# Kernel tuning notes

Measured on AMD Instinct MI355X. Metric: run time of the kernel, lower is better.

The kernel has to match this reference:

```python
import jax, jax.numpy as jnp
import numpy as np
from jax import lax

NPOINT = 1024
NSAMPLE = 64
RADIUS = 0.2
EPS = 1e-5  # BatchNorm eps


def farthest_point_sample(xyz, npoint):
    # xyz: [B, N, 3] -> idx [B, npoint]; deterministic init at point 0
    B, N, _ = xyz.shape

    def step(carry, _):
        dist, farthest = carry
        centroid = jnp.take_along_axis(xyz, farthest[:, None, None], axis=1)  # [B,1,3]
        d = jnp.sum((xyz - centroid) ** 2, axis=-1)  # [B,N]
        dist = jnp.minimum(dist, d)
        new_far = jnp.argmax(dist, axis=-1).astype(jnp.int32)
        return (dist, new_far), farthest

    init = (jnp.full((B, N), 1e10, xyz.dtype), jnp.zeros((B,), jnp.int32))
    _, idxs = lax.scan(step, init, None, length=npoint)
    return jnp.transpose(idxs)  # [B, npoint]


def square_distance(src, dst):
    # src [B,S,3], dst [B,N,3] -> [B,S,N]
    d = -2.0 * jnp.einsum('bsc,bnc->bsn', src, dst)
    d += jnp.sum(src ** 2, -1)[:, :, None]
    d += jnp.sum(dst ** 2, -1)[:, None, :]
    return d


def query_ball_point(radius, nsample, xyz, new_xyz):
    B, N, _ = xyz.shape
    sqr = square_distance(new_xyz, xyz)  # [B,S,N]
    gi = jnp.where(sqr > radius ** 2, N, jnp.arange(N, dtype=jnp.int32))
    gi = jnp.sort(gi, axis=-1)[:, :, :nsample]  # [B,S,K]
    first = gi[:, :, :1]
    gi = jnp.where(gi == N, first, gi)
    return gi


def mlp_bn_relu(x, W, g, b):
    # x [B,S,K,Cin], W [Cin,Cout]; 1x1 conv + training-mode BN + ReLU
    y = jnp.einsum('bskc,co->bsko', x, W)
    m = jnp.mean(y, axis=(0, 1, 2))
    v = jnp.var(y, axis=(0, 1, 2))
    y = (y - m) * lax.rsqrt(v + EPS) * g + b
    return jax.nn.relu(y)


def setup_inputs() -> dict:
    key = jax.random.key(0)
    ks = jax.random.split(key, 8)
    B, N, C = 8, 4096, 128
    xyz = jax.random.uniform(ks[0], (B, N, 3), dtype=jnp.float32)
    features = jax.random.normal(ks[1], (B, C, N), dtype=jnp.float32)
    c_in = C + 3  # use_xyz
    W1 = jax.random.normal(ks[2], (c_in, 128), dtype=jnp.float32) * 0.05
    W2 = jax.random.normal(ks[3], (128, 128), dtype=jnp.float32) * 0.05
    W3 = jax.random.normal(ks[4], (128, 256), dtype=jnp.float32) * 0.05
    return {
        'xyz': xyz, 'features': features,
        'W1': W1, 'g1': jnp.ones((128,)), 'b1': jnp.zeros((128,)),
        'W2': W2, 'g2': jnp.ones((128,)), 'b2': jnp.zeros((128,)),
        'W3': W3, 'g3': jnp.ones((256,)), 'b3': jnp.zeros((256,)),
    }


def reference(xyz, features, W1, g1, b1, W2, g2, b2, W3, g3, b3):
    fps_idx = farthest_point_sample(xyz, NPOINT)              # [B,S]
    new_xyz = jnp.take_along_axis(xyz, fps_idx[:, :, None], axis=1)  # [B,S,3]
    gi = query_ball_point(RADIUS, NSAMPLE, xyz, new_xyz)      # [B,S,K]
    gather = jax.vmap(lambda p, i: p[i])                      # per-batch gather
    grouped_xyz = gather(xyz, gi) - new_xyz[:, :, None, :]    # [B,S,K,3]
    grouped_feat = gather(jnp.transpose(features, (0, 2, 1)), gi)  # [B,S,K,C]
    x = jnp.concatenate([grouped_xyz, grouped_feat], axis=-1)  # [B,S,K,3+C]
    x = mlp_bn_relu(x, W1, g1, b1)
    x = mlp_bn_relu(x, W2, g2, b2)
    x = mlp_bn_relu(x, W3, g3, b3)
    new_features = jnp.transpose(jnp.max(x, axis=2), (0, 2, 1))  # [B,256,S]
    return new_xyz, new_features
```

## Files before the change

### kernel.cpp

```cpp
#include <hip/hip_runtime.h>

#define B_  8
#define N_  4096
#define S_  1024
#define K_  64
#define CF_ 128
#define M_  (B_*S_*K_)

typedef __attribute__((ext_vector_type(8))) short bshort8;
typedef __attribute__((ext_vector_type(4))) float f32x4;
typedef __attribute__((ext_vector_type(4))) int   i32x4;
typedef __attribute__((ext_vector_type(2))) float f32x2;

__device__ __forceinline__ unsigned short f2bf(float f){
  unsigned int u = __float_as_uint(f);
  u = u + 0x7FFFu + ((u >> 16) & 1u);
  return (unsigned short)(u >> 16);
}
__device__ __forceinline__ float bf2f(unsigned short h){
  return __uint_as_float(((unsigned int)h) << 16);
}

#define DPP_PAIR_STEP(CTRL)                                                     \
  {                                                                             \
    int _vi = __builtin_amdgcn_update_dpp(__float_as_int(best), __float_as_int(best), (CTRL), 0xF, 0xF, false); \
    int _ii = __builtin_amdgcn_update_dpp(bidx, bidx, (CTRL), 0xF, 0xF, false); \
    float _ov = __int_as_float(_vi);                                            \
    bool _tk = (_ov > best) || (_ov == best && _ii < bidx);                     \
    best = _tk ? _ov : best;                                                    \
    bidx = _tk ? _ii : bidx;                                                    \
  }

__global__ __launch_bounds__(256) void fps_kernel(const float* __restrict__ xyz,
                                                  float* __restrict__ nx_out,
                                                  float* __restrict__ nx_ws){
#pragma clang fp contract(off)
  __shared__ float sx[N_], sy[N_], sz[N_];
  __shared__ int   sidx[S_];
  __shared__ alignas(16) float redv[2][4];
  __shared__ alignas(16) int   redi[2][4];
  const int b = blockIdx.x, t = threadIdx.x;
  const int lane = t & 63, w = t >> 6;
  const float* xb = xyz + (size_t)b*N_*3;
  f32x2 px[8], py[8], pz[8], dist[8];
#pragma unroll
  for (int j=0;j<8;++j){
    int i0 = (2*j)*256 + t, i1 = (2*j+1)*256 + t;
    float x0=xb[i0*3+0], y0=xb[i0*3+1], z0=xb[i0*3+2];
    float x1=xb[i1*3+0], y1=xb[i1*3+1], z1=xb[i1*3+2];
    px[j] = (f32x2){x0,x1}; py[j] = (f32x2){y0,y1}; pz[j] = (f32x2){z0,z1};
    dist[j] = (f32x2){1e10f,1e10f};
    sx[i0]=x0; sy[i0]=y0; sz[i0]=z0;
    sx[i1]=x1; sy[i1]=y1; sz[i1]=z1;
  }
  __syncthreads();
  int farthest = 0;
  for (int it=0; it<S_; ++it){
    if (t==0) sidx[it] = farthest;
    float cx = sx[farthest], cy = sy[farthest], cz = sz[farthest];
    f32x2 cx2 = (f32x2){cx,cx}, cy2 = (f32x2){cy,cy}, cz2 = (f32x2){cz,cz};
    float best = -1.0f; int bidx = 0;
#pragma unroll
    for (int j=0;j<8;++j){
      f32x2 dx = px[j] - cx2;
      f32x2 dy = py[j] - cy2;
      f32x2 dz = pz[j] - cz2;
      f32x2 d  = (dx*dx + dy*dy) + dz*dz;
      f32x2 nd;
      nd.x = fminf(dist[j].x, d.x);
      nd.y = fminf(dist[j].y, d.y);
      dist[j] = nd;
      bool tk0 = nd.x > best;
      best = tk0 ? nd.x : best;
      bidx = tk0 ? ((2*j)*256 + t) : bidx;
      bool tk1 = nd.y > best;
      best = tk1 ? nd.y : best;
      bidx = tk1 ? ((2*j+1)*256 + t) : bidx;
    }
    DPP_PAIR_STEP(0xB1);
    DPP_PAIR_STEP(0x4E);
    DPP_PAIR_STEP(0x124);
    DPP_PAIR_STEP(0x128);
    DPP_PAIR_STEP(0x142);
    DPP_PAIR_STEP(0x143);
    const int buf = it & 1;
    if (lane == 63){ redv[buf][w] = best; redi[buf][w] = bidx; }
    __syncthreads();
    f32x4 vv = *(const f32x4*)&redv[buf][0];
    i32x4 iv = *(const i32x4*)&redi[buf][0];
    float v01 = vv[0]; int i01 = iv[0];
    { bool tk = (vv[1] > v01) || (vv[1] == v01 && iv[1] < i01); v01 = tk?vv[1]:v01; i01 = tk?iv[1]:i01; }
    float v23 = vv[2]; int i23 = iv[2];
    { bool tk = (vv[3] > v23) || (vv[3] == v23 && iv[3] < i23); v23 = tk?vv[3]:v23; i23 = tk?iv[3]:i23; }
    { bool tk = (v23 > v01) || (v23 == v01 && i23 < i01); v01 = tk?v23:v01; i01 = tk?i23:i01; }
    farthest = i01;
  }
  __syncthreads();
  for (int i=t; i<S_; i+=256){
    int id = sidx[i];
    size_t base = (size_t)(b*S_+i)*3;
    float vx=sx[id], vy=sy[id], vz=sz[id];
    nx_out[base+0]=vx; nx_out[base+1]=vy; nx_out[base+2]=vz;
    nx_ws[base+0]=vx;  nx_ws[base+1]=vy;  nx_ws[base+2]=vz;
  }
}

__global__ __launch_bounds__(256) void qbp_kernel(const float* __restrict__ xyz,
                                                  const float* __restrict__ nx,
                                                  int* __restrict__ gi){
  const double R2 = 0.2*0.2;
  int gtid = blockIdx.x*256 + threadIdx.x;
  int wid = gtid >> 6, lane = gtid & 63;
  int b = wid >> 10, s = wid & 1023;
  const float* xb = xyz + (size_t)b*N_*3;
  const float* c  = nx + (size_t)(b*S_+s)*3;
  double cx=(double)c[0], cy=(double)c[1], cz=(double)c[2];
  double cc = cx*cx + cy*cy + cz*cz;
  int* g = gi + (size_t)(b*S_+s)*K_;
  int count = 0, first = -1;
  for (int ch=0; ch<64 && count<K_; ++ch){
    int i = ch*64 + lane;
    double x = (double)xb[i*3+0], y = (double)xb[i*3+1], z = (double)xb[i*3+2];
    double e  = cx*x + cy*y + cz*z;
    double pp = x*x + y*y + z*z;
    double d  = -2.0*e + cc + pp;
    bool keep = !(d > R2);
    unsigned long long bal = __ballot(keep);
    int pos = count + __builtin_popcountll(bal & ((1ull<<lane)-1ull));
    if (keep && pos < K_) g[pos] = i;
    if (first < 0 && bal) first = ch*64 + (int)__builtin_ctzll(bal);
    count += __builtin_popcountll(bal);
  }
  if (count < K_){
    int p = count + lane;
    if (p < K_) g[p] = first;
  }
}

__global__ __launch_bounds__(256) void transpose_kernel(const float* __restrict__ f,
                                                        unsigned short* __restrict__ ft){
  __shared__ float tile[32][33];
  int b = blockIdx.z, ct = blockIdx.y, nt = blockIdx.x;
  int tx = threadIdx.x & 31, ty = threadIdx.x >> 5;
#pragma unroll
  for (int r=0; r<32; r+=8)
    tile[ty+r][tx] = f[((size_t)(b*128 + ct*32 + ty + r))*4096 + nt*32 + tx];
  __syncthreads();
#pragma unroll
  for (int r=0; r<32; r+=8){
    int n = nt*32 + ty + r, cc = ct*32 + tx;
    ft[((size_t)b*4096 + n)*128 + cc] = f2bf(tile[tx][ty+r]);
  }
}

__global__ void wprep_kernel(const float* __restrict__ W1, const float* __restrict__ W2,
                             const float* __restrict__ W3,
                             unsigned short* __restrict__ Wt1, unsigned short* __restrict__ Wt2,
                             unsigned short* __restrict__ Wt3){
  int t = blockIdx.x*blockDim.x + threadIdx.x;
  int stride = gridDim.x*blockDim.x;
  for (int idx=t; idx<128*160; idx+=stride){
    int n = idx/160, k = idx-(idx/160)*160;
    float v = 0.f;
    if (k < 128) v = W1[(k+3)*128 + n];
    else if (k < 131) v = W1[(k-128)*128 + n];
    Wt1[idx] = f2bf(v);
  }
  for (int idx=t; idx<128*128; idx+=stride){
    int n = idx>>7, k = idx&127;
    Wt2[idx] = f2bf(W2[k*128+n]);
  }
  for (int idx=t; idx<256*128; idx+=stride){
    int n = idx>>7, k = idx&127;
    Wt3[idx] = f2bf(W3[k*256+n]);
  }
}

template<int PHASE>
__global__ __launch_bounds__(256,2) void mm_fused(
    const unsigned short* __restrict__ featT,
    const unsigned short* __restrict__ Wt1,
    const unsigned short* __restrict__ Wt2,
    const unsigned short* __restrict__ Wt3,
    const int* __restrict__ gi,
    const float* __restrict__ xyz,
    const float* __restrict__ nxyz,
    const float* __restrict__ ss1,
    const float* __restrict__ ss2,
    float* __restrict__ slots,
    float* __restrict__ minv,
    float* __restrict__ maxv)
{
  __shared__ alignas(16) unsigned short At[128*40];
  __shared__ alignas(16) unsigned short Bt[128*40];
  __shared__ alignas(16) unsigned short Y[(PHASE>=2)?(128*136):16];
  __shared__ int giL[128];

  const int t = threadIdx.x;
  const int mblk = blockIdx.x;
  const int b = mblk >> 9;
  const int lane = t&63, wave = t>>6;
  const int wm = wave>>1, wn = wave&1;
  const int lrow = lane&15, quad = lane>>4;
  const int slot = mblk & 63;

  if (t<128) giL[t] = gi[(size_t)mblk*128 + t];
  __syncthreads();

  f32x4 acc[4][4];
  const f32x4 z4 = {0.f,0.f,0.f,0.f};
#pragma unroll
  for (int i=0;i<4;++i)
#pragma unroll
    for (int j=0;j<4;++j) acc[i][j]=z4;

  for (int ch=0; ch<5; ++ch){
#pragma unroll
    for (int half=0; half<2; ++half){
      int sl = t + half*256; int r = sl>>2, p = sl&3;
      *(bshort8*)&Bt[r*40+p*8] = *(const bshort8*)(Wt1 + r*160 + ch*32 + p*8);
      if (ch < 4){
        int i = giL[r];
        *(bshort8*)&At[r*40+p*8] =
            *(const bshort8*)(featT + ((size_t)b*N_ + i)*CF_ + ch*32 + p*8);
      } else {
        union { bshort8 v; unsigned short u[8]; } o;
#pragma unroll
        for (int e=0;e<8;++e) o.u[e]=0;
        if (p==0){
          int i = giL[r];
          int s = ((mblk*128 + r) >> 6) & 1023;
          const float* pp = xyz  + ((size_t)b*N_ + i)*3;
          const float* qq = nxyz + (size_t)(b*S_ + s)*3;
          o.u[0] = f2bf(__fsub_rn(pp[0],qq[0]));
          o.u[1] = f2bf(__fsub_rn(pp[1],qq[1]));
          o.u[2] = f2bf(__fsub_rn(pp[2],qq[2]));
        }
        *(bshort8*)&At[r*40+p*8] = o.v;
      }
    }
    __syncthreads();
    bshort8 af[4], bfr[4];
#pragma unroll
    for (int mt=0; mt<4; ++mt) af[mt]  = *(const bshort8*)&At[(wm*64+mt*16+lrow)*40 + quad*8];
#pragma unroll
    for (int nt=0; nt<4; ++nt) bfr[nt] = *(const bshort8*)&Bt[(wn*64+nt*16+lrow)*40 + quad*8];
#pragma unroll
    for (int mt=0; mt<4; ++mt)
#pragma unroll
      for (int nt=0; nt<4; ++nt)
        acc[mt][nt] = __builtin_amdgcn_mfma_f32_16x16x32_bf16(af[mt], bfr[nt], acc[mt][nt], 0,0,0);
    __syncthreads();
  }

  if constexpr (PHASE==1){
#pragma unroll
    for (int nt=0; nt<4; ++nt){
      float s=0.f, s2=0.f;
#pragma unroll
      for (int mt=0; mt<4; ++mt)
#pragma unroll
        for (int r=0; r<4; ++r){ float v=acc[mt][nt][r]; s+=v; s2=fmaf(v,v,s2); }
      s  += __shfl_xor(s,16,64);  s  += __shfl_xor(s,32,64);
      s2 += __shfl_xor(s2,16,64); s2 += __shfl_xor(s2,32,64);
      if (lane<16){
        int c = wn*64+nt*16+lane;
        atomicAdd(&slots[(slot*128+c)*2+0], s);
        atomicAdd(&slots[(slot*128+c)*2+1], s2);
      }
    }
    return;
  }

  if constexpr (PHASE>=2){
#pragma unroll
    for (int nt=0; nt<4; ++nt){
      int c = wn*64+nt*16+lrow;
      float sc = ss1[c], sh = ss1[128+c];
#pragma unroll
      for (int mt=0; mt<4; ++mt)
#pragma unroll
        for (int r=0; r<4; ++r){
          int row = wm*64+mt*16+quad*4+r;
          Y[row*136 + c] = f2bf(fmaxf(fmaf(acc[mt][nt][r], sc, sh), 0.f));
        }
    }
    __syncthreads();

#pragma unroll
    for (int i=0;i<4;++i)
#pragma unroll
      for (int j=0;j<4;++j) acc[i][j]=z4;
    for (int ch=0; ch<4; ++ch){
#pragma unroll
      for (int half=0; half<2; ++half){
        int sl = t + half*256; int r = sl>>2, p = sl&3;
        *(bshort8*)&Bt[r*40+p*8] = *(const bshort8*)(Wt2 + r*128 + ch*32 + p*8);
      }
      __syncthreads();
      bshort8 af[4], bfr[4];
#pragma unroll
      for (int mt=0; mt<4; ++mt) af[mt]  = *(const bshort8*)&Y[(wm*64+mt*16+lrow)*136 + ch*32 + quad*8];
#pragma unroll
      for (int nt=0; nt<4; ++nt) bfr[nt] = *(const bshort8*)&Bt[(wn*64+nt*16+lrow)*40 + quad*8];
#pragma unroll
      for (int mt=0; mt<4; ++mt)
#pragma unroll
        for (int nt=0; nt<4; ++nt)
          acc[mt][nt] = __builtin_amdgcn_mfma_f32_16x16x32_bf16(af[mt], bfr[nt], acc[mt][nt], 0,0,0);
      __syncthreads();
    }
  }

  if constexpr (PHASE==2){
#pragma unroll
    for (int nt=0; nt<4; ++nt){
      float s=0.f, s2=0.f;
#pragma unroll
      for (int mt=0; mt<4; ++mt)
#pragma unroll
        for (int r=0; r<4; ++r){ float v=acc[mt][nt][r]; s+=v; s2=fmaf(v,v,s2); }
      s  += __shfl_xor(s,16,64);  s  += __shfl_xor(s,32,64);
      s2 += __shfl_xor(s2,16,64); s2 += __shfl_xor(s2,32,64);
      if (lane<16){
        int c = wn*64+nt*16+lane;
        atomicAdd(&slots[(slot*128+c)*2+0], s);
        atomicAdd(&slots[(slot*128+c)*2+1], s2);
      }
    }
    return;
  }

  if constexpr (PHASE==3){
#pragma unroll
    for (int nt=0; nt<4; ++nt){
      int c = wn*64+nt*16+lrow;
      float sc = ss2[c], sh = ss2[128+c];
#pragma unroll
      for (int mt=0; mt<4; ++mt)
#pragma unroll
        for (int r=0; r<4; ++r){
          int row = wm*64+mt*16+quad*4+r;
          Y[row*136 + c] = f2bf(fmaxf(fmaf(acc[mt][nt][r], sc, sh), 0.f));
        }
    }
    __syncthreads();

    for (int h=0; h<2; ++h){
#pragma unroll
      for (int i=0;i<4;++i)
#pragma unroll
        for (int j=0;j<4;++j) acc[i][j]=z4;
      for (int ch=0; ch<4; ++ch){
#pragma unroll
        for (int half=0; half<2; ++half){
          int sl = t + half*256; int r = sl>>2, p = sl&3;
          *(bshort8*)&Bt[r*40+p*8] =
              *(const bshort8*)(Wt3 + ((size_t)(h*128+r))*128 + ch*32 + p*8);
        }
        __syncthreads();
        bshort8 af[4], bfr[4];
#pragma unroll
        for (int mt=0; mt<4; ++mt) af[mt]  = *(const bshort8*)&Y[(wm*64+mt*16+lrow)*136 + ch*32 + quad*8];
#pragma unroll
        for (int nt=0; nt<4; ++nt) bfr[nt] = *(const bshort8*)&Bt[(wn*64+nt*16+lrow)*40 + quad*8];
#pragma unroll
        for (int mt=0; mt<4; ++mt)
#pragma unroll
          for (int nt=0; nt<4; ++nt)
            acc[mt][nt] = __builtin_amdgcn_mfma_f32_16x16x32_bf16(af[mt], bfr[nt], acc[mt][nt], 0,0,0);
        __syncthreads();
      }
#pragma unroll
      for (int nt=0; nt<4; ++nt){
        float s=0.f, s2=0.f, mx=-3.0e38f, mn=3.0e38f;
#pragma unroll
        for (int mt=0; mt<4; ++mt)
#pragma unroll
          for (int r=0; r<4; ++r){
            float v=acc[mt][nt][r];
            s+=v; s2=fmaf(v,v,s2);
            mx=fmaxf(mx,v); mn=fminf(mn,v);
          }
        s  += __shfl_xor(s,16,64);  s  += __shfl_xor(s,32,64);
        s2 += __shfl_xor(s2,16,64); s2 += __shfl_xor(s2,32,64);
        mx = fmaxf(mx, __shfl_xor(mx,16,64)); mx = fmaxf(mx, __shfl_xor(mx,32,64));
        mn = fminf(mn, __shfl_xor(mn,16,64)); mn = fminf(mn, __shfl_xor(mn,32,64));
        if (lane<16){
          int c = h*128 + wn*64+nt*16+lane;
          atomicAdd(&slots[(slot*256+c)*2+0], s);
          atomicAdd(&slots[(slot*256+c)*2+1], s2);
          size_t sidx = (size_t)mblk*2 + wm;
          maxv[sidx*256 + c] = mx;
          minv[sidx*256 + c] = mn;
        }
      }
    }
  }
}

__global__ void stats_kernel(const float* __restrict__ slots, const float* __restrict__ g,
                             const float* __restrict__ beta, float* __restrict__ ssOut,
                             int C, float inv_cnt){
  int c = threadIdx.x;
  if (c >= C) return;
  float s=0.f, s2=0.f;
  for (int k=0;k<64;++k){
    s  += slots[(k*C + c)*2 + 0];
    s2 += slots[(k*C + c)*2 + 1];
  }
  float m = s * inv_cnt;
  float v = fmaxf(s2 * inv_cnt - m*m, 0.f);
  float sc = rsqrtf(v + 1e-5f) * g[c];
  ssOut[c] = sc;
  ssOut[C + c] = beta[c] - m*sc;
}

__global__ __launch_bounds__(256) void final_kernel(const float* __restrict__ minv,
                                                    const float* __restrict__ maxv,
                                                    const float* __restrict__ ss3,
                                                    float* __restrict__ out){
  __shared__ float tile[64][65];
  const int t = threadIdx.x;
  const int cb = blockIdx.x;
  const int sb = blockIdx.y;
  const int b  = blockIdx.z;
  const int w = t>>6, l = t&63;
  {
    int c = cb*64 + l;
    float sc = ss3[c], sh = ss3[256+c];
#pragma unroll
    for (int k=0;k<16;++k){
      int sl = k*4 + w;
      size_t mi = ((size_t)(b*1024 + sb*64 + sl))*256 + c;
      float v = (sc >= 0.f) ? maxv[mi] : minv[mi];
      tile[sl][l] = fmaxf(fmaf(v, sc, sh), 0.f);
    }
  }
  __syncthreads();
#pragma unroll
  for (int k=0;k<16;++k){
    int cl = k*4 + w;
    out[((size_t)(b*256 + cb*64 + cl))*1024 + sb*64 + l] = tile[l][cl];
  }
}

extern "C" void kernel_launch(void* const* d_in, const int* in_sizes, int n_in,
                              void* d_out, int out_size, void* d_ws, size_t ws_size,
                              hipStream_t stream){
  const float* xyz      = (const float*)d_in[0];
  const float* features = (const float*)d_in[1];
  const float* W1 = (const float*)d_in[2];
  const float* g1 = (const float*)d_in[3];
  const float* b1 = (const float*)d_in[4];
  const float* W2 = (const float*)d_in[5];
  const float* g2 = (const float*)d_in[6];
  const float* b2 = (const float*)d_in[7];
  const float* W3 = (const float*)d_in[8];
  const float* g3 = (const float*)d_in[9];
  const float* b3 = (const float*)d_in[10];
  float* out = (float*)d_out;

  char* ws = (char*)d_ws;
  size_t off = 0;
  auto alloc = [&](size_t bytes)->char*{
    char* p = ws + off;
    off = (off + bytes + 255) & ~(size_t)255;
    return p;
  };
  float* slots1 = (float*)alloc((size_t)64*128*2*4);
  float* slots2 = (float*)alloc((size_t)64*128*2*4);
  float* slots3 = (float*)alloc((size_t)64*256*2*4);
  float* ss1    = (float*)alloc(256*4);
  float* ss2    = (float*)alloc(256*4);
  float* ss3    = (float*)alloc(512*4);
  float* nxyz   = (float*)alloc((size_t)24576*4);
  int*   gi     = (int*)  alloc((size_t)M_*4);
  unsigned short* featT = (unsigned short*)alloc((size_t)B_*N_*CF_*2);
  unsigned short* Wt1   = (unsigned short*)alloc((size_t)128*160*2);
  unsigned short* Wt2   = (unsigned short*)alloc((size_t)128*128*2);
  unsigned short* Wt3   = (unsigned short*)alloc((size_t)256*128*2);
  float* minv = (float*)alloc((size_t)B_*S_*256*4);
  float* maxv = (float*)alloc((size_t)B_*S_*256*4);

  hipMemsetAsync(slots1, 0, (size_t)(64*128*2 + 64*128*2 + 64*256*2)*4, stream);

  transpose_kernel<<<dim3(128,4,8), 256, 0, stream>>>(features, featT);
  wprep_kernel<<<64, 256, 0, stream>>>(W1, W2, W3, Wt1, Wt2, Wt3);
  fps_kernel<<<8, 256, 0, stream>>>(xyz, out, nxyz);
  qbp_kernel<<<2048, 256, 0, stream>>>(xyz, nxyz, gi);

  const float inv_cnt = 1.0f / (float)M_;
  mm_fused<1><<<4096, 256, 0, stream>>>(featT, Wt1, Wt2, Wt3, gi, xyz, nxyz,
                                        nullptr, nullptr, slots1, nullptr, nullptr);
  stats_kernel<<<1, 128, 0, stream>>>(slots1, g1, b1, ss1, 128, inv_cnt);
  mm_fused<2><<<4096, 256, 0, stream>>>(featT, Wt1, Wt2, Wt3, gi, xyz, nxyz,
                                        ss1, nullptr, slots2, nullptr, nullptr);
  stats_kernel<<<1, 128, 0, stream>>>(slots2, g2, b2, ss2, 128, inv_cnt);
  mm_fused<3><<<4096, 256, 0, stream>>>(featT, Wt1, Wt2, Wt3, gi, xyz, nxyz,
                                        ss1, ss2, slots3, minv, maxv);
  stats_kernel<<<1, 256, 0, stream>>>(slots3, g3, b3, ss3, 256, inv_cnt);
  final_kernel<<<dim3(4,16,8), 256, 0, stream>>>(minv, maxv, ss3, out + 24576);
}
```

Before: 1.168 ms.

## Double-buffer MLP GEMM tiles and carry FPS centroid through reduction

The fused MLP kernels now double-buffer the A and B tiles in shared memory and prefetch the next K-chunk into registers while MFMAs run, which drops one barrier per chunk. The FPS kernel packs xyz as float4 in LDS and reads the four wave-winner coordinates during the final reduction, removing the dependent LDS load of the centroid at the start of each iteration. This doubles tile LDS usage and raises register pressure, and the barrier placement between phases was reworked, so correctness hinges on those syncs.

```diff
diff --git a/kernel.cpp b/kernel.cpp
--- a/kernel.cpp
+++ b/kernel.cpp
@@ -35,7 +35,7 @@
                                                   float* __restrict__ nx_out,
                                                   float* __restrict__ nx_ws){
 #pragma clang fp contract(off)
-  __shared__ float sx[N_], sy[N_], sz[N_];
+  __shared__ alignas(16) float sxyz[N_][4];
   __shared__ int   sidx[S_];
   __shared__ alignas(16) float redv[2][4];
   __shared__ alignas(16) int   redi[2][4];
@@ -50,14 +50,15 @@
     float x1=xb[i1*3+0], y1=xb[i1*3+1], z1=xb[i1*3+2];
     px[j] = (f32x2){x0,x1}; py[j] = (f32x2){y0,y1}; pz[j] = (f32x2){z0,z1};
     dist[j] = (f32x2){1e10f,1e10f};
-    sx[i0]=x0; sy[i0]=y0; sz[i0]=z0;
-    sx[i1]=x1; sy[i1]=y1; sz[i1]=z1;
+    *(f32x4*)&sxyz[i0][0] = (f32x4){x0,y0,z0,0.f};
+    *(f32x4*)&sxyz[i1][0] = (f32x4){x1,y1,z1,0.f};
   }
   __syncthreads();
   int farthest = 0;
+  f32x4 cX = *(const f32x4*)&sxyz[0][0];
+  float cx = cX[0], cy = cX[1], cz = cX[2];
   for (int it=0; it<S_; ++it){
     if (t==0) sidx[it] = farthest;
-    float cx = sx[farthest], cy = sy[farthest], cz = sz[farthest];
     f32x2 cx2 = (f32x2){cx,cx}, cy2 = (f32x2){cy,cy}, cz2 = (f32x2){cz,cz};
     float best = -1.0f; int bidx = 0;
 #pragma unroll
@@ -88,18 +89,25 @@
     __syncthreads();
     f32x4 vv = *(const f32x4*)&redv[buf][0];
     i32x4 iv = *(const i32x4*)&redi[buf][0];
-    float v01 = vv[0]; int i01 = iv[0];
-    { bool tk = (vv[1] > v01) || (vv[1] == v01 && iv[1] < i01); v01 = tk?vv[1]:v01; i01 = tk?iv[1]:i01; }
-    float v23 = vv[2]; int i23 = iv[2];
-    { bool tk = (vv[3] > v23) || (vv[3] == v23 && iv[3] < i23); v23 = tk?vv[3]:v23; i23 = tk?iv[3]:i23; }
-    { bool tk = (v23 > v01) || (v23 == v01 && i23 < i01); v01 = tk?v23:v01; i01 = tk?i23:i01; }
-    farthest = i01;
+    f32x4 p0 = *(const f32x4*)&sxyz[iv[0]][0];
+    f32x4 p1 = *(const f32x4*)&sxyz[iv[1]][0];
+    f32x4 p2 = *(const f32x4*)&sxyz[iv[2]][0];
+    f32x4 p3 = *(const f32x4*)&sxyz[iv[3]][0];
+    bool t1 = (vv[1] > vv[0]) || (vv[1] == vv[0] && iv[1] < iv[0]);
+    float va = t1 ? vv[1] : vv[0]; int ia = t1 ? iv[1] : iv[0];
+    float ax = t1 ? p1[0] : p0[0], ay = t1 ? p1[1] : p0[1], az = t1 ? p1[2] : p0[2];
+    bool t2 = (vv[3] > vv[2]) || (vv[3] == vv[2] && iv[3] < iv[2]);
+    float vb = t2 ? vv[3] : vv[2]; int ib = t2 ? iv[3] : iv[2];
+    float bx = t2 ? p3[0] : p2[0], by = t2 ? p3[1] : p2[1], bz = t2 ? p3[2] : p2[2];
+    bool t3 = (vb > va) || (vb == va && ib < ia);
+    farthest = t3 ? ib : ia;
+    cx = t3 ? bx : ax; cy = t3 ? by : ay; cz = t3 ? bz : az;
   }
   __syncthreads();
   for (int i=t; i<S_; i+=256){
     int id = sidx[i];
     size_t base = (size_t)(b*S_+i)*3;
-    float vx=sx[id], vy=sy[id], vz=sz[id];
+    float vx=sxyz[id][0], vy=sxyz[id][1], vz=sxyz[id][2];
     nx_out[base+0]=vx; nx_out[base+1]=vy; nx_out[base+2]=vz;
     nx_ws[base+0]=vx;  nx_ws[base+1]=vy;  nx_ws[base+2]=vz;
   }
@@ -191,8 +199,8 @@
     float* __restrict__ minv,
     float* __restrict__ maxv)
 {
-  __shared__ alignas(16) unsigned short At[128*40];
-  __shared__ alignas(16) unsigned short Bt[128*40];
+  __shared__ alignas(16) unsigned short At[2][128*40];
+  __shared__ alignas(16) unsigned short Bt[2][128*40];
   __shared__ alignas(16) unsigned short Y[(PHASE>=2)?(128*136):16];
   __shared__ int giL[128];
 
@@ -214,43 +222,70 @@
 #pragma unroll
     for (int j=0;j<4;++j) acc[i][j]=z4;
 
-  for (int ch=0; ch<5; ++ch){
+  {
+    bshort8 aV[2], bV[2];
 #pragma unroll
     for (int half=0; half<2; ++half){
       int sl = t + half*256; int r = sl>>2, p = sl&3;
-      *(bshort8*)&Bt[r*40+p*8] = *(const bshort8*)(Wt1 + r*160 + ch*32 + p*8);
+      bV[half] = *(const bshort8*)(Wt1 + r*160 + p*8);
+      int i = giL[r];
+      aV[half] = *(const bshort8*)(featT + ((size_t)b*N_ + i)*CF_ + p*8);
+    }
+#pragma unroll
+    for (int half=0; half<2; ++half){
+      int sl = t + half*256; int r = sl>>2, p = sl&3;
+      *(bshort8*)&At[0][r*40+p*8] = aV[half];
+      *(bshort8*)&Bt[0][r*40+p*8] = bV[half];
+    }
+    for (int ch=0; ch<5; ++ch){
+      const int cur = ch & 1;
+      __syncthreads();
+      bshort8 af[4], bfr[4];
+#pragma unroll
+      for (int mt=0; mt<4; ++mt) af[mt]  = *(const bshort8*)&At[cur][(wm*64+mt*16+lrow)*40 + quad*8];
+#pragma unroll
+      for (int nt=0; nt<4; ++nt) bfr[nt] = *(const bshort8*)&Bt[cur][(wn*64+nt*16+lrow)*40 + quad*8];
       if (ch < 4){
-        int i = giL[r];
-        *(bshort8*)&At[r*40+p*8] =
-            *(const bshort8*)(featT + ((size_t)b*N_ + i)*CF_ + ch*32 + p*8);
-      } else {
-        union { bshort8 v; unsigned short u[8]; } o;
-#pragma unroll
-        for (int e=0;e<8;++e) o.u[e]=0;
-        if (p==0){
-          int i = giL[r];
-          int s = ((mblk*128 + r) >> 6) & 1023;
-          const float* pp = xyz  + ((size_t)b*N_ + i)*3;
-          const float* qq = nxyz + (size_t)(b*S_ + s)*3;
-          o.u[0] = f2bf(__fsub_rn(pp[0],qq[0]));
-          o.u[1] = f2bf(__fsub_rn(pp[1],qq[1]));
-          o.u[2] = f2bf(__fsub_rn(pp[2],qq[2]));
-        }
-        *(bshort8*)&At[r*40+p*8] = o.v;
-      }
-    }
-    __syncthreads();
-    bshort8 af[4], bfr[4];
-#pragma unroll
-    for (int mt=0; mt<4; ++mt) af[mt]  = *(const bshort8*)&At[(wm*64+mt*16+lrow)*40 + quad*8];
-#pragma unroll
-    for (int nt=0; nt<4; ++nt) bfr[nt] = *(const bshort8*)&Bt[(wn*64+nt*16+lrow)*40 + quad*8];
-#pragma unroll
-    for (int mt=0; mt<4; ++mt)
-#pragma unroll
-      for (int nt=0; nt<4; ++nt)
-        acc[mt][nt] = __builtin_amdgcn_mfma_f32_16x16x32_bf16(af[mt], bfr[nt], acc[mt][nt], 0,0,0);
-    __syncthreads();
+        const int nch = ch + 1;
+#pragma unroll
+        for (int half=0; half<2; ++half){
+          int sl = t + half*256; int r = sl>>2, p = sl&3;
+          bV[half] = *(const bshort8*)(Wt1 + r*160 + nch*32 + p*8);
+          if (nch < 4){
+            int i = giL[r];
+            aV[half] = *(const bshort8*)(featT + ((size_t)b*N_ + i)*CF_ + nch*32 + p*8);
+          } else {
+            union { bshort8 v; unsigned short u[8]; } o;
+#pragma unroll
+            for (int e=0;e<8;++e) o.u[e]=0;
+            if (p==0){
+              int i = giL[r];
+              int s = ((mblk*128 + r) >> 6) & 1023;
+              const float* pp = xyz  + ((size_t)b*N_ + i)*3;
+              const float* qq = nxyz + (size_t)(b*S_ + s)*3;
+              o.u[0] = f2bf(__fsub_rn(pp[0],qq[0]));
+              o.u[1] = f2bf(__fsub_rn(pp[1],qq[1]));
+              o.u[2] = f2bf(__fsub_rn(pp[2],qq[2]));
+            }
+            aV[half] = o.v;
+          }
+        }
+      }
+#pragma unroll
+      for (int mt=0; mt<4; ++mt)
+#pragma unroll
+        for (int nt=0; nt<4; ++nt)
+          acc[mt][nt] = __builtin_amdgcn_mfma_f32_16x16x32_bf16(af[mt], bfr[nt], acc[mt][nt], 0,0,0);
+      if (ch < 4){
+        const int nxt = cur ^ 1;
+#pragma unroll
+        for (int half=0; half<2; ++half){
+          int sl = t + half*256; int r = sl>>2, p = sl&3;
+          *(bshort8*)&At[nxt][r*40+p*8] = aV[half];
+          *(bshort8*)&Bt[nxt][r*40+p*8] = bV[half];
+        }
+      }
+    }
   }
 
   if constexpr (PHASE==1){
@@ -285,30 +320,52 @@
           Y[row*136 + c] = f2bf(fmaxf(fmaf(acc[mt][nt][r], sc, sh), 0.f));
         }
     }
-    __syncthreads();
 
 #pragma unroll
     for (int i=0;i<4;++i)
 #pragma unroll
       for (int j=0;j<4;++j) acc[i][j]=z4;
-    for (int ch=0; ch<4; ++ch){
+    {
+      bshort8 bV[2];
 #pragma unroll
       for (int half=0; half<2; ++half){
         int sl = t + half*256; int r = sl>>2, p = sl&3;
-        *(bshort8*)&Bt[r*40+p*8] = *(const bshort8*)(Wt2 + r*128 + ch*32 + p*8);
-      }
-      __syncthreads();
-      bshort8 af[4], bfr[4];
-#pragma unroll
-      for (int mt=0; mt<4; ++mt) af[mt]  = *(const bshort8*)&Y[(wm*64+mt*16+lrow)*136 + ch*32 + quad*8];
-#pragma unroll
-      for (int nt=0; nt<4; ++nt) bfr[nt] = *(const bshort8*)&Bt[(wn*64+nt*16+lrow)*40 + quad*8];
-#pragma unroll
-      for (int mt=0; mt<4; ++mt)
-#pragma unroll
-        for (int nt=0; nt<4; ++nt)
-          acc[mt][nt] = __builtin_amdgcn_mfma_f32_16x16x32_bf16(af[mt], bfr[nt], acc[mt][nt], 0,0,0);
-      __syncthreads();
+        bV[half] = *(const bshort8*)(Wt2 + r*128 + p*8);
+      }
+#pragma unroll
+      for (int half=0; half<2; ++half){
+        int sl = t + half*256; int r = sl>>2, p = sl&3;
+        *(bshort8*)&Bt[1][r*40+p*8] = bV[half];
+      }
+      for (int ch=0; ch<4; ++ch){
+        const int cur = (ch & 1) ^ 1;
+        __syncthreads();
+        bshort8 af[4], bfr[4];
+#pragma unroll
+        for (int mt=0; mt<4; ++mt) af[mt]  = *(const bshort8*)&Y[(wm*64+mt*16+lrow)*136 + ch*32 + quad*8];
+#pragma unroll
+        for (int nt=0; nt<4; ++nt) bfr[nt] = *(const bshort8*)&Bt[cur][(wn*64+nt*16+lrow)*40 + quad*8];
+        if (ch < 3){
+#pragma unroll
+          for (int half=0; half<2; ++half){
+            int sl = t + half*256; int r = sl>>2, p = sl&3;
+            bV[half] = *(const bshort8*)(Wt2 + r*128 + (ch+1)*32 + p*8);
+          }
+        }
+#pragma unroll
+        for (int mt=0; mt<4; ++mt)
+#pragma unroll
+          for (int nt=0; nt<4; ++nt)
+            acc[mt][nt] = __builtin_amdgcn_mfma_f32_16x16x32_bf16(af[mt], bfr[nt], acc[mt][nt], 0,0,0);
+        if (ch < 3){
+          const int nxt = cur ^ 1;
+#pragma unroll
+          for (int half=0; half<2; ++half){
+            int sl = t + half*256; int r = sl>>2, p = sl&3;
+            *(bshort8*)&Bt[nxt][r*40+p*8] = bV[half];
+          }
+        }
+      }
     }
   }
 
@@ -332,6 +389,7 @@
   }
 
   if constexpr (PHASE==3){
+    __syncthreads();
 #pragma unroll
     for (int nt=0; nt<4; ++nt){
       int c = wn*64+nt*16+lrow;
@@ -344,32 +402,51 @@
           Y[row*136 + c] = f2bf(fmaxf(fmaf(acc[mt][nt][r], sc, sh), 0.f));
         }
     }
-    __syncthreads();
 
     for (int h=0; h<2; ++h){
 #pragma unroll
       for (int i=0;i<4;++i)
 #pragma unroll
         for (int j=0;j<4;++j) acc[i][j]=z4;
+      bshort8 bV[2];
+#pragma unroll
+      for (int half=0; half<2; ++half){
+        int sl = t + half*256; int r = sl>>2, p = sl&3;
+        bV[half] = *(const bshort8*)(Wt3 + ((size_t)(h*128+r))*128 + p*8);
+      }
+#pragma unroll
+      for (int half=0; half<2; ++half){
+        int sl = t + half*256; int r = sl>>2, p = sl&3;
+        *(bshort8*)&Bt[1][r*40+p*8] = bV[half];
+      }
       for (int ch=0; ch<4; ++ch){
-#pragma unroll
-        for (int half=0; half<2; ++half){
-          int sl = t + half*256; int r = sl>>2, p = sl&3;
-          *(bshort8*)&Bt[r*40+p*8] =
-              *(const bshort8*)(Wt3 + ((size_t)(h*128+r))*128 + ch*32 + p*8);
-        }
+        const int cur = (ch & 1) ^ 1;
         __syncthreads();
         bshort8 af[4], bfr[4];
 #pragma unroll
         for (int mt=0; mt<4; ++mt) af[mt]  = *(const bshort8*)&Y[(wm*64+mt*16+lrow)*136 + ch*32 + quad*8];
 #pragma unroll
-        for (int nt=0; nt<4; ++nt) bfr[nt] = *(const bshort8*)&Bt[(wn*64+nt*16+lrow)*40 + quad*8];
+        for (int nt=0; nt<4; ++nt) bfr[nt] = *(const bshort8*)&Bt[cur][(wn*64+nt*16+lrow)*40 + quad*8];
+        if (ch < 3){
+#pragma unroll
+          for (int half=0; half<2; ++half){
+            int sl = t + half*256; int r = sl>>2, p = sl&3;
+            bV[half] = *(const bshort8*)(Wt3 + ((size_t)(h*128+r))*128 + (ch+1)*32 + p*8);
+          }
+        }
 #pragma unroll
         for (int mt=0; mt<4; ++mt)
 #pragma unroll
           for (int nt=0; nt<4; ++nt)
             acc[mt][nt] = __builtin_amdgcn_mfma_f32_16x16x32_bf16(af[mt], bfr[nt], acc[mt][nt], 0,0,0);
-        __syncthreads();
+        if (ch < 3){
+          const int nxt = cur ^ 1;
+#pragma unroll
+          for (int half=0; half<2; ++half){
+            int sl = t + half*256; int r = sl>>2, p = sl&3;
+            *(bshort8*)&Bt[nxt][r*40+p*8] = bV[half];
+          }
+        }
       }
 #pragma unroll
       for (int nt=0; nt<4; ++nt){
```

Result: slower. 1.191 ms (+2.0%).

## Precompute per-point first-layer projection and gather it instead of grouped features

Applied to the files above, without the earlier changes.

The first 1x1 conv is applied once per input point (B*N rows) in a new pgemm kernel, producing a float projection P. The three fused phases then gather P rows and add the xyz-offset term with FMAs instead of gathering 128-channel features and running a K=160 MFMA GEMM per grouped row. This removes roughly 64x redundant layer-1 work, but the gather now moves fp32 rows, doubling bytes per gathered element compared with bf16. The layer-2 and layer-3 weight tiles also get double-buffered LDS staging with register prefetch, and layer-1 statistics are reduced in LDS before the global atomics.

```diff
diff --git a/kernel.cpp b/kernel.cpp
--- a/kernel.cpp
+++ b/kernel.cpp
@@ -11,6 +11,7 @@
 typedef __attribute__((ext_vector_type(4))) float f32x4;
 typedef __attribute__((ext_vector_type(4))) int   i32x4;
 typedef __attribute__((ext_vector_type(2))) float f32x2;
+typedef __attribute__((ext_vector_type(4))) unsigned short us4;
 
 __device__ __forceinline__ unsigned short f2bf(float f){
   unsigned int u = __float_as_uint(f);
@@ -176,10 +177,58 @@
   }
 }
 
+__global__ __launch_bounds__(256,2) void pgemm_kernel(const unsigned short* __restrict__ featT,
+                                                      const unsigned short* __restrict__ Wt1,
+                                                      float* __restrict__ P){
+  __shared__ alignas(16) unsigned short At[128*40];
+  __shared__ alignas(16) unsigned short Bt[128*40];
+  const int t = threadIdx.x, blk = blockIdx.x;
+  const size_t rowBase = (size_t)blk*128;
+  const int lane = t&63, wave = t>>6;
+  const int wm = wave>>1, wn = wave&1;
+  const int lrow = lane&15, quad = lane>>4;
+  f32x4 acc[4][4];
+  const f32x4 z4 = {0.f,0.f,0.f,0.f};
+#pragma unroll
+  for (int i=0;i<4;++i)
+#pragma unroll
+    for (int j=0;j<4;++j) acc[i][j]=z4;
+  for (int ch=0; ch<4; ++ch){
+    __syncthreads();
+#pragma unroll
+    for (int half=0; half<2; ++half){
+      int sl = t + half*256; int r = sl>>2, p = sl&3;
+      *(bshort8*)&At[r*40+p*8] = *(const bshort8*)(featT + (rowBase + r)*CF_ + ch*32 + p*8);
+      *(bshort8*)&Bt[r*40+p*8] = *(const bshort8*)(Wt1 + r*160 + ch*32 + p*8);
+    }
+    __syncthreads();
+    bshort8 af[4], bfr[4];
+#pragma unroll
+    for (int mt=0; mt<4; ++mt) af[mt]  = *(const bshort8*)&At[(wm*64+mt*16+lrow)*40 + quad*8];
+#pragma unroll
+    for (int nt=0; nt<4; ++nt) bfr[nt] = *(const bshort8*)&Bt[(wn*64+nt*16+lrow)*40 + quad*8];
+#pragma unroll
+    for (int mt=0; mt<4; ++mt)
+#pragma unroll
+      for (int nt=0; nt<4; ++nt)
+        acc[mt][nt] = __builtin_amdgcn_mfma_f32_16x16x32_bf16(af[mt], bfr[nt], acc[mt][nt], 0,0,0);
+  }
+#pragma unroll
+  for (int mt=0; mt<4; ++mt)
+#pragma unroll
+    for (int nt=0; nt<4; ++nt)
+#pragma unroll
+      for (int r=0; r<4; ++r){
+        int row = wm*64 + mt*16 + quad*4 + r;
+        int col = wn*64 + nt*16 + lrow;
+        P[(rowBase + row)*128 + col] = acc[mt][nt][r];
+      }
+}
+
 template<int PHASE>
 __global__ __launch_bounds__(256,2) void mm_fused(
-    const unsigned short* __restrict__ featT,
-    const unsigned short* __restrict__ Wt1,
+    const float* __restrict__ P,
+    const float* __restrict__ W1,
     const unsigned short* __restrict__ Wt2,
     const unsigned short* __restrict__ Wt3,
     const int* __restrict__ gi,
@@ -191,10 +240,12 @@
     float* __restrict__ minv,
     float* __restrict__ maxv)
 {
-  __shared__ alignas(16) unsigned short At[128*40];
-  __shared__ alignas(16) unsigned short Bt[128*40];
+  __shared__ alignas(16) unsigned short Bt[2][(PHASE>=2)?(128*40):8];
   __shared__ alignas(16) unsigned short Y[(PHASE>=2)?(128*136):16];
   __shared__ int giL[128];
+  __shared__ alignas(16) float dxL[128][4];
+  __shared__ alignas(16) float w0L[128], w1L[128], w2L[128];
+  __shared__ float sLDS[(PHASE==1)?128:4], s2LDS[(PHASE==1)?128:4];
 
   const int t = threadIdx.x;
   const int mblk = blockIdx.x;
@@ -204,195 +255,220 @@
   const int lrow = lane&15, quad = lane>>4;
   const int slot = mblk & 63;
 
-  if (t<128) giL[t] = gi[(size_t)mblk*128 + t];
+  if (t<128){
+    int i = gi[(size_t)mblk*128 + t];
+    giL[t] = i;
+    int s = ((mblk*128 + t) >> 6) & 1023;
+    const float* pp = xyz  + ((size_t)b*N_ + i)*3;
+    const float* qq = nxyz + (size_t)(b*S_ + s)*3;
+    dxL[t][0] = __fsub_rn(pp[0],qq[0]);
+    dxL[t][1] = __fsub_rn(pp[1],qq[1]);
+    dxL[t][2] = __fsub_rn(pp[2],qq[2]);
+    w0L[t] = W1[t]; w1L[t] = W1[128+t]; w2L[t] = W1[256+t];
+    if constexpr (PHASE==1){ sLDS[t]=0.f; s2LDS[t]=0.f; }
+  }
   __syncthreads();
 
-  f32x4 acc[4][4];
-  const f32x4 z4 = {0.f,0.f,0.f,0.f};
-#pragma unroll
-  for (int i=0;i<4;++i)
-#pragma unroll
-    for (int j=0;j<4;++j) acc[i][j]=z4;
-
-  for (int ch=0; ch<5; ++ch){
-#pragma unroll
-    for (int half=0; half<2; ++half){
-      int sl = t + half*256; int r = sl>>2, p = sl&3;
-      *(bshort8*)&Bt[r*40+p*8] = *(const bshort8*)(Wt1 + r*160 + ch*32 + p*8);
-      if (ch < 4){
-        int i = giL[r];
-        *(bshort8*)&At[r*40+p*8] =
-            *(const bshort8*)(featT + ((size_t)b*N_ + i)*CF_ + ch*32 + p*8);
+  {
+    const int rgrp = t>>5, cq = (t&31)*4;
+    f32x4 w0 = *(const f32x4*)&w0L[cq];
+    f32x4 w1 = *(const f32x4*)&w1L[cq];
+    f32x4 w2 = *(const f32x4*)&w2L[cq];
+    f32x4 a1v, b1v;
+    if constexpr (PHASE>=2){
+      a1v = *(const f32x4*)(ss1 + cq);
+      b1v = *(const f32x4*)(ss1 + 128 + cq);
+    }
+    f32x4 sA = {0,0,0,0}, s2A = {0,0,0,0};
+#pragma unroll
+    for (int g=0; g<16; ++g){
+      int r = g*8 + rgrp;
+      int pi = giL[r];
+      f32x4 p = *(const f32x4*)(P + ((size_t)b*N_ + pi)*128 + cq);
+      float dx = dxL[r][0], dy = dxL[r][1], dz = dxL[r][2];
+      f32x4 y;
+#pragma unroll
+      for (int e=0;e<4;++e)
+        y[e] = fmaf(dz, w2[e], fmaf(dy, w1[e], fmaf(dx, w0[e], p[e])));
+      if constexpr (PHASE==1){
+#pragma unroll
+        for (int e=0;e<4;++e){ sA[e] += y[e]; s2A[e] = fmaf(y[e], y[e], s2A[e]); }
       } else {
-        union { bshort8 v; unsigned short u[8]; } o;
-#pragma unroll
-        for (int e=0;e<8;++e) o.u[e]=0;
-        if (p==0){
-          int i = giL[r];
-          int s = ((mblk*128 + r) >> 6) & 1023;
-          const float* pp = xyz  + ((size_t)b*N_ + i)*3;
-          const float* qq = nxyz + (size_t)(b*S_ + s)*3;
-          o.u[0] = f2bf(__fsub_rn(pp[0],qq[0]));
-          o.u[1] = f2bf(__fsub_rn(pp[1],qq[1]));
-          o.u[2] = f2bf(__fsub_rn(pp[2],qq[2]));
-        }
-        *(bshort8*)&At[r*40+p*8] = o.v;
-      }
-    }
-    __syncthreads();
-    bshort8 af[4], bfr[4];
-#pragma unroll
-    for (int mt=0; mt<4; ++mt) af[mt]  = *(const bshort8*)&At[(wm*64+mt*16+lrow)*40 + quad*8];
-#pragma unroll
-    for (int nt=0; nt<4; ++nt) bfr[nt] = *(const bshort8*)&Bt[(wn*64+nt*16+lrow)*40 + quad*8];
-#pragma unroll
-    for (int mt=0; mt<4; ++mt)
-#pragma unroll
-      for (int nt=0; nt<4; ++nt)
-        acc[mt][nt] = __builtin_amdgcn_mfma_f32_16x16x32_bf16(af[mt], bfr[nt], acc[mt][nt], 0,0,0);
-    __syncthreads();
-  }
-
-  if constexpr (PHASE==1){
-#pragma unroll
-    for (int nt=0; nt<4; ++nt){
-      float s=0.f, s2=0.f;
-#pragma unroll
-      for (int mt=0; mt<4; ++mt)
-#pragma unroll
-        for (int r=0; r<4; ++r){ float v=acc[mt][nt][r]; s+=v; s2=fmaf(v,v,s2); }
-      s  += __shfl_xor(s,16,64);  s  += __shfl_xor(s,32,64);
-      s2 += __shfl_xor(s2,16,64); s2 += __shfl_xor(s2,32,64);
-      if (lane<16){
-        int c = wn*64+nt*16+lane;
-        atomicAdd(&slots[(slot*128+c)*2+0], s);
-        atomicAdd(&slots[(slot*128+c)*2+1], s2);
-      }
-    }
-    return;
+        us4 zz;
+#pragma unroll
+        for (int e=0;e<4;++e)
+          zz[e] = f2bf(fmaxf(fmaf(y[e], a1v[e], b1v[e]), 0.f));
+        *(us4*)&Y[r*136 + cq] = zz;
+      }
+    }
+    if constexpr (PHASE==1){
+#pragma unroll
+      for (int e=0;e<4;++e){
+        atomicAdd(&sLDS[cq+e],  sA[e]);
+        atomicAdd(&s2LDS[cq+e], s2A[e]);
+      }
+      __syncthreads();
+      if (t<128){
+        atomicAdd(&slots[(slot*128+t)*2+0], sLDS[t]);
+        atomicAdd(&slots[(slot*128+t)*2+1], s2LDS[t]);
+      }
+      return;
+    }
   }
 
   if constexpr (PHASE>=2){
-#pragma unroll
-    for (int nt=0; nt<4; ++nt){
-      int c = wn*64+nt*16+lrow;
-      float sc = ss1[c], sh = ss1[128+c];
-#pragma unroll
-      for (int mt=0; mt<4; ++mt)
-#pragma unroll
-        for (int r=0; r<4; ++r){
-          int row = wm*64+mt*16+quad*4+r;
-          Y[row*136 + c] = f2bf(fmaxf(fmaf(acc[mt][nt][r], sc, sh), 0.f));
-        }
-    }
-    __syncthreads();
-
+    f32x4 acc[4][4];
+    const f32x4 z4 = {0.f,0.f,0.f,0.f};
 #pragma unroll
     for (int i=0;i<4;++i)
 #pragma unroll
       for (int j=0;j<4;++j) acc[i][j]=z4;
-    for (int ch=0; ch<4; ++ch){
+
+    {
+      bshort8 bV[2];
 #pragma unroll
       for (int half=0; half<2; ++half){
         int sl = t + half*256; int r = sl>>2, p = sl&3;
-        *(bshort8*)&Bt[r*40+p*8] = *(const bshort8*)(Wt2 + r*128 + ch*32 + p*8);
-      }
+        bV[half] = *(const bshort8*)(Wt2 + r*128 + p*8);
+      }
+#pragma unroll
+      for (int half=0; half<2; ++half){
+        int sl = t + half*256; int r = sl>>2, p = sl&3;
+        *(bshort8*)&Bt[1][r*40+p*8] = bV[half];
+      }
+      for (int ch=0; ch<4; ++ch){
+        const int cur = (ch & 1) ^ 1;
+        __syncthreads();
+        bshort8 af[4], bfr[4];
+#pragma unroll
+        for (int mt=0; mt<4; ++mt) af[mt]  = *(const bshort8*)&Y[(wm*64+mt*16+lrow)*136 + ch*32 + quad*8];
+#pragma unroll
+        for (int nt=0; nt<4; ++nt) bfr[nt] = *(const bshort8*)&Bt[cur][(wn*64+nt*16+lrow)*40 + quad*8];
+        if (ch < 3){
+#pragma unroll
+          for (int half=0; half<2; ++half){
+            int sl = t + half*256; int r = sl>>2, p = sl&3;
+            bV[half] = *(const bshort8*)(Wt2 + r*128 + (ch+1)*32 + p*8);
+          }
+        }
+#pragma unroll
+        for (int mt=0; mt<4; ++mt)
+#pragma unroll
+          for (int nt=0; nt<4; ++nt)
+            acc[mt][nt] = __builtin_amdgcn_mfma_f32_16x16x32_bf16(af[mt], bfr[nt], acc[mt][nt], 0,0,0);
+        if (ch < 3){
+          const int nxt = cur ^ 1;
+#pragma unroll
+          for (int half=0; half<2; ++half){
+            int sl = t + half*256; int r = sl>>2, p = sl&3;
+            *(bshort8*)&Bt[nxt][r*40+p*8] = bV[half];
+          }
+        }
+      }
+    }
+
+    if constexpr (PHASE==2){
+#pragma unroll
+      for (int nt=0; nt<4; ++nt){
+        float s=0.f, s2=0.f;
+#pragma unroll
+        for (int mt=0; mt<4; ++mt)
+#pragma unroll
+          for (int r=0; r<4; ++r){ float v=acc[mt][nt][r]; s+=v; s2=fmaf(v,v,s2); }
+        s  += __shfl_xor(s,16,64);  s  += __shfl_xor(s,32,64);
+        s2 += __shfl_xor(s2,16,64); s2 += __shfl_xor(s2,32,64);
+        if (lane<16){
+          int c = wn*64+nt*16+lane;
+          atomicAdd(&slots[(slot*128+c)*2+0], s);
+          atomicAdd(&slots[(slot*128+c)*2+1], s2);
+        }
+      }
+      return;
+    }
+
+    if constexpr (PHASE==3){
       __syncthreads();
-      bshort8 af[4], bfr[4];
-#pragma unroll
-      for (int mt=0; mt<4; ++mt) af[mt]  = *(const bshort8*)&Y[(wm*64+mt*16+lrow)*136 + ch*32 + quad*8];
-#pragma unroll
-      for (int nt=0; nt<4; ++nt) bfr[nt] = *(const bshort8*)&Bt[(wn*64+nt*16+lrow)*40 + quad*8];
-#pragma unroll
-      for (int mt=0; mt<4; ++mt)
-#pragma unroll
-        for (int nt=0; nt<4; ++nt)
-          acc[mt][nt] = __builtin_amdgcn_mfma_f32_16x16x32_bf16(af[mt], bfr[nt], acc[mt][nt], 0,0,0);
-      __syncthreads();
-    }
-  }
-
-  if constexpr (PHASE==2){
-#pragma unroll
-    for (int nt=0; nt<4; ++nt){
-      float s=0.f, s2=0.f;
-#pragma unroll
-      for (int mt=0; mt<4; ++mt)
-#pragma unroll
-        for (int r=0; r<4; ++r){ float v=acc[mt][nt][r]; s+=v; s2=fmaf(v,v,s2); }
-      s  += __shfl_xor(s,16,64);  s  += __shfl_xor(s,32,64);
-      s2 += __shfl_xor(s2,16,64); s2 += __shfl_xor(s2,32,64);
-      if (lane<16){
-        int c = wn*64+nt*16+lane;
-        atomicAdd(&slots[(slot*128+c)*2+0], s);
-        atomicAdd(&slots[(slot*128+c)*2+1], s2);
-      }
-    }
-    return;
-  }
-
-  if constexpr (PHASE==3){
-#pragma unroll
-    for (int nt=0; nt<4; ++nt){
-      int c = wn*64+nt*16+lrow;
-      float sc = ss2[c], sh = ss2[128+c];
-#pragma unroll
-      for (int mt=0; mt<4; ++mt)
-#pragma unroll
-        for (int r=0; r<4; ++r){
-          int row = wm*64+mt*16+quad*4+r;
-          Y[row*136 + c] = f2bf(fmaxf(fmaf(acc[mt][nt][r], sc, sh), 0.f));
-        }
-    }
-    __syncthreads();
-
-    for (int h=0; h<2; ++h){
-#pragma unroll
-      for (int i=0;i<4;++i)
-#pragma unroll
-        for (int j=0;j<4;++j) acc[i][j]=z4;
-      for (int ch=0; ch<4; ++ch){
+#pragma unroll
+      for (int nt=0; nt<4; ++nt){
+        int c = wn*64+nt*16+lrow;
+        float sc = ss2[c], sh = ss2[128+c];
+#pragma unroll
+        for (int mt=0; mt<4; ++mt)
+#pragma unroll
+          for (int r=0; r<4; ++r){
+            int row = wm*64+mt*16+quad*4+r;
+            Y[row*136 + c] = f2bf(fmaxf(fmaf(acc[mt][nt][r], sc, sh), 0.f));
+          }
+      }
+
+      for (int h=0; h<2; ++h){
+#pragma unroll
+        for (int i=0;i<4;++i)
+#pragma unroll
+          for (int j=0;j<4;++j) acc[i][j]=z4;
+        bshort8 bV[2];
 #pragma unroll
         for (int half=0; half<2; ++half){
           int sl = t + half*256; int r = sl>>2, p = sl&3;
-          *(bshort8*)&Bt[r*40+p*8] =
-              *(const bshort8*)(Wt3 + ((size_t)(h*128+r))*128 + ch*32 + p*8);
-        }
-        __syncthreads();
-        bshort8 af[4], bfr[4];
-#pragma unroll
-        for (int mt=0; mt<4; ++mt) af[mt]  = *(const bshort8*)&Y[(wm*64+mt*16+lrow)*136 + ch*32 + quad*8];
-#pragma unroll
-        for (int nt=0; nt<4; ++nt) bfr[nt] = *(const bshort8*)&Bt[(wn*64+nt*16+lrow)*40 + quad*8];
-#pragma unroll
-        for (int mt=0; mt<4; ++mt)
-#pragma unroll
-          for (int nt=0; nt<4; ++nt)
-            acc[mt][nt] = __builtin_amdgcn_mfma_f32_16x16x32_bf16(af[mt], bfr[nt], acc[mt][nt], 0,0,0);
-        __syncthreads();
-      }
-#pragma unroll
-      for (int nt=0; nt<4; ++nt){
-        float s=0.f, s2=0.f, mx=-3.0e38f, mn=3.0e38f;
-#pragma unroll
-        for (int mt=0; mt<4; ++mt)
-#pragma unroll
-          for (int r=0; r<4; ++r){
-            float v=acc[mt][nt][r];
-            s+=v; s2=fmaf(v,v,s2);
-            mx=fmaxf(mx,v); mn=fminf(mn,v);
+          bV[half] = *(const bshort8*)(Wt3 + ((size_t)(h*128+r))*128 + p*8);
+        }
+#pragma unroll
+        for (int half=0; half<2; ++half){
+          int sl = t + half*256; int r = sl>>2, p = sl&3;
+          *(bshort8*)&Bt[1][r*40+p*8] = bV[half];
+        }
+        for (int ch=0; ch<4; ++ch){
+          const int cur = (ch & 1) ^ 1;
+          __syncthreads();
+          bshort8 af[4], bfr[4];
+#pragma unroll
+          for (int mt=0; mt<4; ++mt) af[mt]  = *(const bshort8*)&Y[(wm*64+mt*16+lrow)*136 + ch*32 + quad*8];
+#pragma unroll
+          for (int nt=0; nt<4; ++nt) bfr[nt] = *(const bshort8*)&Bt[cur][(wn*64+nt*16+lrow)*40 + quad*8];
+          if (ch < 3){
+#pragma unroll
+            for (int half=0; half<2; ++half){
+              int sl = t + half*256; int r = sl>>2, p = sl&3;
+              bV[half] = *(const bshort8*)(Wt3 + ((size_t)(h*128+r))*128 + (ch+1)*32 + p*8);
+            }
           }
-        s  += __shfl_xor(s,16,64);  s  += __shfl_xor(s,32,64);
-        s2 += __shfl_xor(s2,16,64); s2 += __shfl_xor(s2,32,64);
-        mx = fmaxf(mx, __shfl_xor(mx,16,64)); mx = fmaxf(mx, __shfl_xor(mx,32,64));
-        mn = fminf(mn, __shfl_xor(mn,16,64)); mn = fminf(mn, __shfl_xor(mn,32,64));
-        if (lane<16){
-          int c = h*128 + wn*64+nt*16+lane;
-          atomicAdd(&slots[(slot*256+c)*2+0], s);
-          atomicAdd(&slots[(slot*256+c)*2+1], s2);
-          size_t sidx = (size_t)mblk*2 + wm;
-          maxv[sidx*256 + c] = mx;
-          minv[sidx*256 + c] = mn;
+#pragma unroll
+          for (int mt=0; mt<4; ++mt)
+#pragma unroll
+            for (int nt=0; nt<4; ++nt)
+              acc[mt][nt] = __builtin_amdgcn_mfma_f32_16x16x32_bf16(af[mt], bfr[nt], acc[mt][nt], 0,0,0);
+          if (ch < 3){
+            const int nxt = cur ^ 1;
+#pragma unroll
+            for (int half=0; half<2; ++half){
+              int sl = t + half*256; int r = sl>>2, p = sl&3;
+              *(bshort8*)&Bt[nxt][r*40+p*8] = bV[half];
+            }
+          }
+        }
+#pragma unroll
+        for (int nt=0; nt<4; ++nt){
+          float s=0.f, s2=0.f, mx=-3.0e38f, mn=3.0e38f;
+#pragma unroll
+          for (int mt=0; mt<4; ++mt)
+#pragma unroll
+            for (int r=0; r<4; ++r){
+              float v=acc[mt][nt][r];
+              s+=v; s2=fmaf(v,v,s2);
+              mx=fmaxf(mx,v); mn=fminf(mn,v);
+            }
+          s  += __shfl_xor(s,16,64);  s  += __shfl_xor(s,32,64);
+          s2 += __shfl_xor(s2,16,64); s2 += __shfl_xor(s2,32,64);
+          mx = fmaxf(mx, __shfl_xor(mx,16,64)); mx = fmaxf(mx, __shfl_xor(mx,32,64));
+          mn = fminf(mn, __shfl_xor(mn,16,64)); mn = fminf(mn, __shfl_xor(mn,32,64));
+          if (lane<16){
+            int c = h*128 + wn*64+nt*16+lane;
+            atomicAdd(&slots[(slot*256+c)*2+0], s);
+            atomicAdd(&slots[(slot*256+c)*2+1], s2);
+            size_t sidx = (size_t)mblk*2 + wm;
+            maxv[sidx*256 + c] = mx;
+            minv[sidx*256 + c] = mn;
+          }
         }
       }
     }
@@ -482,22 +558,24 @@
   unsigned short* Wt3   = (unsigned short*)alloc((size_t)256*128*2);
   float* minv = (float*)alloc((size_t)B_*S_*256*4);
   float* maxv = (float*)alloc((size_t)B_*S_*256*4);
+  float* P    = (float*)alloc((size_t)B_*N_*128*4);
 
   hipMemsetAsync(slots1, 0, (size_t)(64*128*2 + 64*128*2 + 64*256*2)*4, stream);
 
   transpose_kernel<<<dim3(128,4,8), 256, 0, stream>>>(features, featT);
   wprep_kernel<<<64, 256, 0, stream>>>(W1, W2, W3, Wt1, Wt2, Wt3);
+  pgemm_kernel<<<256, 256, 0, stream>>>(featT, Wt1, P);
   fps_kernel<<<8, 256, 0, stream>>>(xyz, out, nxyz);
   qbp_kernel<<<2048, 256, 0, stream>>>(xyz, nxyz, gi);
 
   const float inv_cnt = 1.0f / (float)M_;
-  mm_fused<1><<<4096, 256, 0, stream>>>(featT, Wt1, Wt2, Wt3, gi, xyz, nxyz,
+  mm_fused<1><<<4096, 256, 0, stream>>>(P, W1, Wt2, Wt3, gi, xyz, nxyz,
                                         nullptr, nullptr, slots1, nullptr, nullptr);
   stats_kernel<<<1, 128, 0, stream>>>(slots1, g1, b1, ss1, 128, inv_cnt);
-  mm_fused<2><<<4096, 256, 0, stream>>>(featT, Wt1, Wt2, Wt3, gi, xyz, nxyz,
+  mm_fused<2><<<4096, 256, 0, stream>>>(P, W1, Wt2, Wt3, gi, xyz, nxyz,
                                         ss1, nullptr, slots2, nullptr, nullptr);
   stats_kernel<<<1, 128, 0, stream>>>(slots2, g2, b2, ss2, 128, inv_cnt);
-  mm_fused<3><<<4096, 256, 0, stream>>>(featT, Wt1, Wt2, Wt3, gi, xyz, nxyz,
+  mm_fused<3><<<4096, 256, 0, stream>>>(P, W1, Wt2, Wt3, gi, xyz, nxyz,
                                         ss1, ss2, slots3, minv, maxv);
   stats_kernel<<<1, 256, 0, stream>>>(slots3, g3, b3, ss3, 256, inv_cnt);
   final_kernel<<<dim3(4,16,8), 256, 0, stream>>>(minv, maxv, ss3, out + 24576);
```

Result: faster. 1.144 ms (-2.0%).
